# Optimization experiments

Measured on AMD Instinct MI355X. Metric: run time of the kernel, lower is better.

## Reference

```python
import jax, jax.numpy as jnp
import numpy as np

N = 100000   # nodes
E = 1600000  # edges per relation (avg in-degree 16)
D = 128      # gcn_hidden (in_feat == out_feat)
R = 2        # relations: forward_edge, backward_edge


def setup_inputs() -> dict:
    key = jax.random.key(0)
    ks = jax.random.split(key, 8)
    x = jax.random.normal(ks[0], (N, D), dtype=jnp.float32)
    src_fwd = jax.random.randint(ks[1], (E,), 0, N, dtype=jnp.int32)
    dst_fwd = jax.random.randint(ks[2], (E,), 0, N, dtype=jnp.int32)
    src_bwd = jax.random.randint(ks[3], (E,), 0, N, dtype=jnp.int32)
    dst_bwd = jax.random.randint(ks[4], (E,), 0, N, dtype=jnp.int32)
    # xavier_uniform with relu gain sqrt(2)
    gain = np.sqrt(2.0)
    lim_rel = gain * np.sqrt(6.0 / (D + D))
    rel_weight = jax.random.uniform(ks[5], (R, D, D), minval=-lim_rel, maxval=lim_rel, dtype=jnp.float32)
    loop_weight = jax.random.uniform(ks[6], (D, D), minval=-lim_rel, maxval=lim_rel, dtype=jnp.float32)
    h_bias = jnp.zeros((D,), dtype=jnp.float32)
    return {
        'x': x,
        'src_fwd': src_fwd, 'dst_fwd': dst_fwd,
        'src_bwd': src_bwd, 'dst_bwd': dst_bwd,
        'rel_weight': rel_weight, 'loop_weight': loop_weight, 'h_bias': h_bias,
    }


def _rel_conv(x, src, dst, W):
    # dgl GraphConv(norm='right', weight per relation): scatter-sum src feats to
    # dst, divide by clamped in-degree, then matmul W (in_feat == out_feat so
    # order of matmul vs aggregation is mathematically equivalent).
    msg = x[src]                                            # [E, D] gather
    agg = jax.ops.segment_sum(msg, dst, num_segments=N)     # [N, D] scatter-add
    deg = jax.ops.segment_sum(jnp.ones((src.shape[0],), x.dtype), dst, num_segments=N)
    agg = agg / jnp.clip(deg, 1.0)[:, None]                 # right norm, deg clamp(min=1)
    return agg @ W                                          # [N, D]


def reference(x, src_fwd, dst_fwd, src_bwd, dst_bwd, rel_weight, loop_weight, h_bias):
    h = _rel_conv(x, src_fwd, dst_fwd, rel_weight[0])
    h = h + _rel_conv(x, src_bwd, dst_bwd, rel_weight[1])   # HeteroGraphConv sums per-relation results
    h = h + x @ loop_weight                                 # self loop
    h = h + h_bias                                          # bias
    h = jax.nn.relu(h)                                      # activation
    return h                                                # dropout is identity in eval
```

## Files before the change

### kernel.cpp

```cpp
#include <hip/hip_runtime.h>
#include <hip/hip_bf16.h>


#define DFEAT 128
#define CH2 16384
#define PSH 6
#define NBMAX 3200
#define CAPB 1536
#define CAPP 1792
#define NPACK 24

typedef __attribute__((ext_vector_type(8))) short short8v;
typedef __attribute__((ext_vector_type(4))) float float4v;
typedef __attribute__((ext_vector_type(4))) unsigned int uint4v;
typedef __attribute__((ext_vector_type(4))) unsigned short ushort4v;

__global__ __launch_bounds__(256) void front_kernel(
        const float4v* __restrict__ x4, ushort4v* __restrict__ xb4, int n4,
        const int* __restrict__ src0, const int* __restrict__ dst0,
        const int* __restrict__ src1, const int* __restrict__ dst1,
        int* __restrict__ cursor, unsigned* __restrict__ binned,
        const float* __restrict__ wrel, const float* __restrict__ wloop,
        unsigned short* __restrict__ wb,
        int N, int E, int nbin) {
    __shared__ int cnt[NBMAX];
    __shared__ int base[NBMAX];
    int tid = threadIdx.x;
    int bid = blockIdx.x;

    if (bid < nbin) {
        for (int i = tid; i < NBMAX; i += 256) cnt[i] = 0;
        __syncthreads();
        int lo = bid * CH2, hi = min(2 * E, lo + CH2);
        for (int i = lo + tid; i < hi; i += 256) {
            int r = (i >= E) ? 1 : 0;
            int e = i - r * E;
            int t = r ? dst1[e] : dst0[e];
            atomicAdd(&cnt[(r * N + t) >> PSH], 1);
        }
        __syncthreads();
        for (int b = tid; b < NBMAX; b += 256) {
            int c = cnt[b];
            if (c) base[b] = b * CAPB + atomicAdd(&cursor[b], c);
        }
        __syncthreads();
        for (int i = lo + tid; i < hi; i += 256) {
            int r = (i >= E) ? 1 : 0;
            int e = i - r * E;
            int s = r ? src1[e] : src0[e];
            int t = r ? dst1[e] : dst0[e];
            int p = r * N + t;
            int slot = atomicAdd(&base[p >> PSH], 1);
            binned[slot] = ((unsigned)(p & 63) << 17) | (unsigned)s;
        }
    } else if (bid < nbin + NPACK) {
        int t = (bid - nbin) * 256 + tid;
        if (t < 12 * 8 * 64) {
            int lane = t & 63;
            int kbase = (t >> 9) * 32 + (lane >> 4) * 8;
            int col = (((t >> 6) & 7) << 4) + (lane & 15);
            unsigned short tmp[8];
#pragma unroll
            for (int j = 0; j < 8; ++j) {
                int k = kbase + j;
                float v = (k < 256) ? wrel[k * DFEAT + col]
                                    : wloop[(k - 256) * DFEAT + col];
                tmp[j] = __hip_bfloat16_raw(__float2bfloat16(v)).x;
            }
            *(ushort4*)(wb + t * 8)     = make_ushort4(tmp[0], tmp[1], tmp[2], tmp[3]);
            *(ushort4*)(wb + t * 8 + 4) = make_ushort4(tmp[4], tmp[5], tmp[6], tmp[7]);
        }
    } else {
        int cb = bid - nbin - NPACK;
        int i = cb * 256 + tid;
        if (i < n4) {
            float4v v = __builtin_nontemporal_load(x4 + i);
            ushort4v o;
            o[0] = __hip_bfloat16_raw(__float2bfloat16(v[0])).x;
            o[1] = __hip_bfloat16_raw(__float2bfloat16(v[1])).x;
            o[2] = __hip_bfloat16_raw(__float2bfloat16(v[2])).x;
            o[3] = __hip_bfloat16_raw(__float2bfloat16(v[3])).x;
            xb4[i] = o;
        }
        if (cb == 0 && tid < 32) {
            ushort4v z = (ushort4v){0, 0, 0, 0};
            xb4[n4 + tid] = z;
        }
    }
}

__global__ __launch_bounds__(256) void agg_kernel(
        const unsigned short* __restrict__ xb,
        const unsigned* __restrict__ binned,
        const int* __restrict__ cursor,
        unsigned short* __restrict__ aggb, int N, int M) {
    __shared__ unsigned ebuf[CAPP];
    __shared__ int cnt[64], cur[64], rs[64];
    int tid = threadIdx.x;
    int b = blockIdx.x;
    int total = min(cursor[b], CAPB);
    const unsigned* seg = binned + (size_t)b * CAPB;
    int P0 = b << PSH;
    unsigned SENT = (unsigned)N << 8;

    if (tid < 64) cnt[tid] = 0;
    for (int i = tid; i < CAPP; i += 256) ebuf[i] = SENT;
    __syncthreads();
    for (int i = tid; i < total; i += 256)
        atomicAdd(&cnt[seg[i] >> 17], 1);
    __syncthreads();
    if (tid < 64) {
        int c = cnt[tid];
        int cp = (c + 3) & ~3;
        int inc = cp;
#pragma unroll
        for (int off = 1; off < 64; off <<= 1) {
            int t2 = __shfl_up(inc, off);
            if (tid >= off) inc += t2;
        }
        rs[tid] = inc - cp;
        cur[tid] = inc - cp;
    }
    __syncthreads();
    for (int i = tid; i < total; i += 256) {
        unsigned v = seg[i];
        int slot = atomicAdd(&cur[v >> 17], 1);
        ebuf[slot] = (v & 0x1FFFF) << 8;
    }
    __syncthreads();

    int wv = tid >> 6, lane = tid & 63;
    int lq = lane >> 4;
    int lb = (lane & 15) << 4;
    const char* xbB = (const char*)xb;

#define ACCUM(Q) {                                          \
        A0[0] += __uint_as_float(Q[0] << 16);               \
        A0[1] += __uint_as_float(Q[0] & 0xffff0000u);       \
        A0[2] += __uint_as_float(Q[1] << 16);               \
        A0[3] += __uint_as_float(Q[1] & 0xffff0000u);       \
        A1[0] += __uint_as_float(Q[2] << 16);               \
        A1[1] += __uint_as_float(Q[2] & 0xffff0000u);       \
        A1[2] += __uint_as_float(Q[3] << 16);               \
        A1[3] += __uint_as_float(Q[3] & 0xffff0000u); }

    for (int pi = 0; pi < 16; ++pi) {
        int pl = wv * 16 + pi;
        int s0 = rs[pl], c = cnt[pl];
        int ng = (c + 3) >> 2;
        float4v A0 = (float4v){0.f, 0.f, 0.f, 0.f};
        float4v A1 = (float4v){0.f, 0.f, 0.f, 0.f};
        if (ng > 0) {
            uint4v c0, c1, nx;
            { unsigned off = ebuf[s0 + lq];
              c0 = *(const uint4v*)(xbB + off + lb); }
            if (ng > 1) {
                unsigned off = ebuf[s0 + 4 + lq];
                c1 = *(const uint4v*)(xbB + off + lb);
            }
            for (int g = 2; g < ng; ++g) {
                { unsigned off = ebuf[s0 + 4 * g + lq];
                  nx = *(const uint4v*)(xbB + off + lb); }
                ACCUM(c0);
                c0 = c1; c1 = nx;
            }
            ACCUM(c0);
            if (ng > 1) ACCUM(c1);
        }
#pragma unroll
        for (int j = 0; j < 4; ++j) {
            A0[j] += __shfl_xor(A0[j], 16);
            A0[j] += __shfl_xor(A0[j], 32);
            A1[j] += __shfl_xor(A1[j], 16);
            A1[j] += __shfl_xor(A1[j], 32);
        }
        int pg = P0 + pl;
        if (pg < M && lane < 16) {
            float inv = 1.0f / (float)max(c, 1);
            ushort4v w0, w1;
            w0[0] = __hip_bfloat16_raw(__float2bfloat16(A0[0] * inv)).x;
            w0[1] = __hip_bfloat16_raw(__float2bfloat16(A0[1] * inv)).x;
            w0[2] = __hip_bfloat16_raw(__float2bfloat16(A0[2] * inv)).x;
            w0[3] = __hip_bfloat16_raw(__float2bfloat16(A0[3] * inv)).x;
            w1[0] = __hip_bfloat16_raw(__float2bfloat16(A1[0] * inv)).x;
            w1[1] = __hip_bfloat16_raw(__float2bfloat16(A1[1] * inv)).x;
            w1[2] = __hip_bfloat16_raw(__float2bfloat16(A1[2] * inv)).x;
            w1[3] = __hip_bfloat16_raw(__float2bfloat16(A1[3] * inv)).x;
            unsigned short* dst = aggb + (size_t)pg * DFEAT + lane * 8;
            __builtin_nontemporal_store(w0, (ushort4v*)dst);
            __builtin_nontemporal_store(w1, (ushort4v*)(dst + 4));
        }
    }
#undef ACCUM
}

__global__ __launch_bounds__(256) void mfma_gemm_kernel(
        const unsigned short* __restrict__ aggb,
        const unsigned short* __restrict__ xb,
        const unsigned short* __restrict__ wb,
        const float* __restrict__ bias,
        float* __restrict__ out, int N) {
    int tid = threadIdx.x;
    int wv = tid >> 6, lane = tid & 63;
    int R0 = blockIdx.x * 128 + wv * 32;
    int mrow = lane & 15, quad = lane >> 4;

    float4v acc[2][8];
#pragma unroll
    for (int rt = 0; rt < 2; ++rt)
#pragma unroll
        for (int ct = 0; ct < 8; ++ct) acc[rt][ct] = (float4v){0.f, 0.f, 0.f, 0.f};

    int n0 = min(R0 + mrow, N - 1);
    int n1 = min(R0 + 16 + mrow, N - 1);

#pragma unroll
    for (int kc = 0; kc < 12; ++kc) {
        int off = (kc & 3) * 32 + quad * 8;
        const unsigned short* s0;
        const unsigned short* s1;
        if (kc < 4)      { s0 = aggb + (size_t)n0 * DFEAT;       s1 = aggb + (size_t)n1 * DFEAT; }
        else if (kc < 8) { s0 = aggb + (size_t)(N + n0) * DFEAT; s1 = aggb + (size_t)(N + n1) * DFEAT; }
        else             { s0 = xb + (size_t)n0 * DFEAT;         s1 = xb + (size_t)n1 * DFEAT; }
        short8v a0 = *(const short8v*)(s0 + off);
        short8v a1 = *(const short8v*)(s1 + off);
#pragma unroll
        for (int ct = 0; ct < 8; ++ct) {
            short8v bfr = *(const short8v*)(wb + (((kc * 8 + ct) << 6) + lane) * 8);
            acc[0][ct] = __builtin_amdgcn_mfma_f32_16x16x32_bf16(a0, bfr, acc[0][ct], 0, 0, 0);
            acc[1][ct] = __builtin_amdgcn_mfma_f32_16x16x32_bf16(a1, bfr, acc[1][ct], 0, 0, 0);
        }
    }

#pragma unroll
    for (int ct = 0; ct < 8; ++ct) {
        int col = ct * 16 + mrow;
        float bv = bias[col];
#pragma unroll
        for (int rt = 0; rt < 2; ++rt) {
#pragma unroll
            for (int i = 0; i < 4; ++i) {
                int row = R0 + rt * 16 + quad * 4 + i;
                if (row < N)
                    __builtin_nontemporal_store(fmaxf(acc[rt][ct][i] + bv, 0.f),
                                                out + (size_t)row * DFEAT + col);
            }
        }
    }
}

extern "C" void kernel_launch(void* const* d_in, const int* in_sizes, int n_in,
                              void* d_out, int out_size, void* d_ws, size_t ws_size,
                              hipStream_t stream) {
    const float* x      = (const float*)d_in[0];
    const int* src_fwd  = (const int*)d_in[1];
    const int* dst_fwd  = (const int*)d_in[2];
    const int* src_bwd  = (const int*)d_in[3];
    const int* dst_bwd  = (const int*)d_in[4];
    const float* wrel   = (const float*)d_in[5];
    const float* wloop  = (const float*)d_in[6];
    const float* hbias  = (const float*)d_in[7];
    float* out          = (float*)d_out;

    int N = in_sizes[0] / DFEAT;
    int E = in_sizes[1];
    int M = 2 * N;
    int TE = 2 * E;
    int NB = (M + 63) / 64;

    unsigned short* wb   = (unsigned short*)d_ws;
    unsigned* binned     = (unsigned*)(wb + 12 * 8 * 64 * 8);
    unsigned short* xb   = (unsigned short*)(binned + (size_t)NB * CAPB);
    unsigned short* aggb = xb + (size_t)(N + 1) * DFEAT;
    int* cursor          = (int*)(aggb + (size_t)M * DFEAT);

    int n4 = N * (DFEAT / 4);
    int nconv = (n4 + 255) / 256;
    int nbin = (TE + CH2 - 1) / CH2;

    hipMemsetAsync(cursor, 0, NB * sizeof(int), stream);

    front_kernel<<<nbin + NPACK + nconv, 256, 0, stream>>>(
        (const float4v*)x, (ushort4v*)xb, n4,
        src_fwd, dst_fwd, src_bwd, dst_bwd,
        cursor, binned, wrel, wloop, wb, N, E, nbin);

    agg_kernel<<<NB, 256, 0, stream>>>(xb, binned, cursor, aggb, N, M);

    mfma_gemm_kernel<<<(N + 127) / 128, 256, 0, stream>>>(
        aggb, xb, wb, hbias, out, N);
}
```

Baseline: 378.4 us.

## Restructure aggregation to half-wave per row with 4-edge unrolled gathers

The aggregation kernel moves from 64-lane waves, where each quarter-wave gathered a different edge and partial sums were combined by shuffles, to 32-lane groups in 128-thread blocks. Each lane now loads 8 bytes of every neighbour row, and the loop handles four edges at a time with a scalar tail. This drops the sentinel padding of edge lists, the zero-row padding write and the cross-lane shuffle reduction. The cost is narrower 8-byte loads per lane and a split between unrolled loop and tail; fewer threads per block also changes occupancy and LDS use.

Result: faster. 366.7 us (-3.1%).

```diff
diff --git a/kernel.cpp b/kernel.cpp
--- a/kernel.cpp
+++ b/kernel.cpp
@@ -7,12 +7,11 @@
 #define PSH 6
 #define NBMAX 3200
 #define CAPB 1536
-#define CAPP 1792
 #define NPACK 24
 
 typedef __attribute__((ext_vector_type(8))) short short8v;
 typedef __attribute__((ext_vector_type(4))) float float4v;
-typedef __attribute__((ext_vector_type(4))) unsigned int uint4v;
+typedef __attribute__((ext_vector_type(2))) unsigned int u2v;
 typedef __attribute__((ext_vector_type(4))) unsigned short ushort4v;
 
 __global__ __launch_bounds__(256) void front_kernel(
@@ -82,116 +81,109 @@
             o[3] = __hip_bfloat16_raw(__float2bfloat16(v[3])).x;
             xb4[i] = o;
         }
-        if (cb == 0 && tid < 32) {
-            ushort4v z = (ushort4v){0, 0, 0, 0};
-            xb4[n4 + tid] = z;
-        }
-    }
-}
-
-__global__ __launch_bounds__(256) void agg_kernel(
-        const unsigned short* __restrict__ xb,
+    }
+}
+
+__global__ __launch_bounds__(128) void agg_kernel(
+        const u2v* __restrict__ xb2,
         const unsigned* __restrict__ binned,
         const int* __restrict__ cursor,
         unsigned short* __restrict__ aggb, int N, int M) {
-    __shared__ unsigned ebuf[CAPP];
+    __shared__ unsigned ebuf[CAPB];
     __shared__ int cnt[64], cur[64], rs[64];
     int tid = threadIdx.x;
     int b = blockIdx.x;
     int total = min(cursor[b], CAPB);
     const unsigned* seg = binned + (size_t)b * CAPB;
     int P0 = b << PSH;
-    unsigned SENT = (unsigned)N << 8;
+    int hw = tid >> 5, lane = tid & 31;
 
     if (tid < 64) cnt[tid] = 0;
-    for (int i = tid; i < CAPP; i += 256) ebuf[i] = SENT;
-    __syncthreads();
-    for (int i = tid; i < total; i += 256)
+    __syncthreads();
+    for (int i = tid; i < total; i += 128)
         atomicAdd(&cnt[seg[i] >> 17], 1);
     __syncthreads();
     if (tid < 64) {
         int c = cnt[tid];
-        int cp = (c + 3) & ~3;
-        int inc = cp;
+        int inc = c;
 #pragma unroll
         for (int off = 1; off < 64; off <<= 1) {
             int t2 = __shfl_up(inc, off);
             if (tid >= off) inc += t2;
         }
-        rs[tid] = inc - cp;
-        cur[tid] = inc - cp;
-    }
-    __syncthreads();
-    for (int i = tid; i < total; i += 256) {
+        rs[tid] = inc - c;
+        cur[tid] = inc - c;
+    }
+    __syncthreads();
+    for (int i = tid; i < total; i += 128) {
         unsigned v = seg[i];
         int slot = atomicAdd(&cur[v >> 17], 1);
-        ebuf[slot] = (v & 0x1FFFF) << 8;
-    }
-    __syncthreads();
-
-    int wv = tid >> 6, lane = tid & 63;
-    int lq = lane >> 4;
-    int lb = (lane & 15) << 4;
-    const char* xbB = (const char*)xb;
-
-#define ACCUM(Q) {                                          \
-        A0[0] += __uint_as_float(Q[0] << 16);               \
-        A0[1] += __uint_as_float(Q[0] & 0xffff0000u);       \
-        A0[2] += __uint_as_float(Q[1] << 16);               \
-        A0[3] += __uint_as_float(Q[1] & 0xffff0000u);       \
-        A1[0] += __uint_as_float(Q[2] << 16);               \
-        A1[1] += __uint_as_float(Q[2] & 0xffff0000u);       \
-        A1[2] += __uint_as_float(Q[3] << 16);               \
-        A1[3] += __uint_as_float(Q[3] & 0xffff0000u); }
+        ebuf[slot] = v & 0x1FFFFu;
+    }
+    __syncthreads();
 
     for (int pi = 0; pi < 16; ++pi) {
-        int pl = wv * 16 + pi;
+        int pl = hw * 16 + pi;
         int s0 = rs[pl], c = cnt[pl];
-        int ng = (c + 3) >> 2;
-        float4v A0 = (float4v){0.f, 0.f, 0.f, 0.f};
-        float4v A1 = (float4v){0.f, 0.f, 0.f, 0.f};
-        if (ng > 0) {
-            uint4v c0, c1, nx;
-            { unsigned off = ebuf[s0 + lq];
-              c0 = *(const uint4v*)(xbB + off + lb); }
-            if (ng > 1) {
-                unsigned off = ebuf[s0 + 4 + lq];
-                c1 = *(const uint4v*)(xbB + off + lb);
+        float4v a = (float4v){0.f, 0.f, 0.f, 0.f};
+        int e = 0;
+        if (c >= 4) {
+            int sA = ebuf[s0];
+            int sB = ebuf[s0 + 1];
+            int sC = ebuf[s0 + 2];
+            int sD = ebuf[s0 + 3];
+            u2v cAq = xb2[(size_t)sA * 32 + lane];
+            u2v cBq = xb2[(size_t)sB * 32 + lane];
+            u2v cCq = xb2[(size_t)sC * 32 + lane];
+            u2v cDq = xb2[(size_t)sD * 32 + lane];
+            for (e = 4; e + 4 <= c; e += 4) {
+                int nA = ebuf[s0 + e];
+                int nB = ebuf[s0 + e + 1];
+                int nC = ebuf[s0 + e + 2];
+                int nD = ebuf[s0 + e + 3];
+                u2v gA = xb2[(size_t)nA * 32 + lane];
+                u2v gB = xb2[(size_t)nB * 32 + lane];
+                u2v gC = xb2[(size_t)nC * 32 + lane];
+                u2v gD = xb2[(size_t)nD * 32 + lane];
+                a[0] += __uint_as_float(cAq[0] << 16) + __uint_as_float(cBq[0] << 16)
+                      + __uint_as_float(cCq[0] << 16) + __uint_as_float(cDq[0] << 16);
+                a[1] += __uint_as_float(cAq[0] & 0xffff0000u) + __uint_as_float(cBq[0] & 0xffff0000u)
+                      + __uint_as_float(cCq[0] & 0xffff0000u) + __uint_as_float(cDq[0] & 0xffff0000u);
+                a[2] += __uint_as_float(cAq[1] << 16) + __uint_as_float(cBq[1] << 16)
+                      + __uint_as_float(cCq[1] << 16) + __uint_as_float(cDq[1] << 16);
+                a[3] += __uint_as_float(cAq[1] & 0xffff0000u) + __uint_as_float(cBq[1] & 0xffff0000u)
+                      + __uint_as_float(cCq[1] & 0xffff0000u) + __uint_as_float(cDq[1] & 0xffff0000u);
+                cAq = gA; cBq = gB; cCq = gC; cDq = gD;
             }
-            for (int g = 2; g < ng; ++g) {
-                { unsigned off = ebuf[s0 + 4 * g + lq];
-                  nx = *(const uint4v*)(xbB + off + lb); }
-                ACCUM(c0);
-                c0 = c1; c1 = nx;
-            }
-            ACCUM(c0);
-            if (ng > 1) ACCUM(c1);
-        }
-#pragma unroll
-        for (int j = 0; j < 4; ++j) {
-            A0[j] += __shfl_xor(A0[j], 16);
-            A0[j] += __shfl_xor(A0[j], 32);
-            A1[j] += __shfl_xor(A1[j], 16);
-            A1[j] += __shfl_xor(A1[j], 32);
+            a[0] += __uint_as_float(cAq[0] << 16) + __uint_as_float(cBq[0] << 16)
+                  + __uint_as_float(cCq[0] << 16) + __uint_as_float(cDq[0] << 16);
+            a[1] += __uint_as_float(cAq[0] & 0xffff0000u) + __uint_as_float(cBq[0] & 0xffff0000u)
+                  + __uint_as_float(cCq[0] & 0xffff0000u) + __uint_as_float(cDq[0] & 0xffff0000u);
+            a[2] += __uint_as_float(cAq[1] << 16) + __uint_as_float(cBq[1] << 16)
+                  + __uint_as_float(cCq[1] << 16) + __uint_as_float(cDq[1] << 16);
+            a[3] += __uint_as_float(cAq[1] & 0xffff0000u) + __uint_as_float(cBq[1] & 0xffff0000u)
+                  + __uint_as_float(cCq[1] & 0xffff0000u) + __uint_as_float(cDq[1] & 0xffff0000u);
+        }
+        for (; e < c; ++e) {
+            int s = ebuf[s0 + e];
+            u2v g = xb2[(size_t)s * 32 + lane];
+            a[0] += __uint_as_float(g[0] << 16);
+            a[1] += __uint_as_float(g[0] & 0xffff0000u);
+            a[2] += __uint_as_float(g[1] << 16);
+            a[3] += __uint_as_float(g[1] & 0xffff0000u);
         }
         int pg = P0 + pl;
-        if (pg < M && lane < 16) {
+        if (pg < M) {
             float inv = 1.0f / (float)max(c, 1);
-            ushort4v w0, w1;
-            w0[0] = __hip_bfloat16_raw(__float2bfloat16(A0[0] * inv)).x;
-            w0[1] = __hip_bfloat16_raw(__float2bfloat16(A0[1] * inv)).x;
-            w0[2] = __hip_bfloat16_raw(__float2bfloat16(A0[2] * inv)).x;
-            w0[3] = __hip_bfloat16_raw(__float2bfloat16(A0[3] * inv)).x;
-            w1[0] = __hip_bfloat16_raw(__float2bfloat16(A1[0] * inv)).x;
-            w1[1] = __hip_bfloat16_raw(__float2bfloat16(A1[1] * inv)).x;
-            w1[2] = __hip_bfloat16_raw(__float2bfloat16(A1[2] * inv)).x;
-            w1[3] = __hip_bfloat16_raw(__float2bfloat16(A1[3] * inv)).x;
-            unsigned short* dst = aggb + (size_t)pg * DFEAT + lane * 8;
-            __builtin_nontemporal_store(w0, (ushort4v*)dst);
-            __builtin_nontemporal_store(w1, (ushort4v*)(dst + 4));
-        }
-    }
-#undef ACCUM
+            ushort4v w;
+            w[0] = __hip_bfloat16_raw(__float2bfloat16(a[0] * inv)).x;
+            w[1] = __hip_bfloat16_raw(__float2bfloat16(a[1] * inv)).x;
+            w[2] = __hip_bfloat16_raw(__float2bfloat16(a[2] * inv)).x;
+            w[3] = __hip_bfloat16_raw(__float2bfloat16(a[3] * inv)).x;
+            __builtin_nontemporal_store(
+                w, (ushort4v*)(aggb + (size_t)pg * DFEAT + 4 * lane));
+        }
+    }
 }
 
 __global__ __launch_bounds__(256) void mfma_gemm_kernel(
@@ -278,14 +270,15 @@
     int nconv = (n4 + 255) / 256;
     int nbin = (TE + CH2 - 1) / CH2;
 
-    hipMemsetAsync(cursor, 0, NB * sizeof(int), stream);
+    (void)hipMemsetAsync(cursor, 0, NB * sizeof(int), stream);
 
     front_kernel<<<nbin + NPACK + nconv, 256, 0, stream>>>(
         (const float4v*)x, (ushort4v*)xb, n4,
         src_fwd, dst_fwd, src_bwd, dst_bwd,
         cursor, binned, wrel, wloop, wb, N, E, nbin);
 
-    agg_kernel<<<NB, 256, 0, stream>>>(xb, binned, cursor, aggb, N, M);
+    agg_kernel<<<NB, 128, 0, stream>>>(
+        (const u2v*)xb, binned, cursor, aggb, N, M);
 
     mfma_gemm_kernel<<<(N + 127) / 128, 256, 0, stream>>>(
         aggb, xb, wb, hbias, out, N);
```
